# Kernel optimization log

Hardware: AMD Instinct MI355X
Metric: run time of the kernel (lower is better)

Reference implementation:

```python
import jax, jax.numpy as jnp
import numpy as np

N = 50000   # nodes
R = 4       # relation groups
E = 800000  # nnz per relation adjacency
ED = 200000 # decoded edges
H = 128     # hidden_dim
L = 64      # latent_dim
DH = 64     # decoder_hidden_dim


def setup_inputs() -> dict:
    key = jax.random.key(0)
    ks = iter(jax.random.split(key, 64))
    def nrm(shape, scale=1.0):
        return jax.random.normal(next(ks), shape, dtype=jnp.float32) * scale
    inp = {}
    inp["x_process"] = nrm((N, 62))
    inp["x_file"] = nrm((N, 37))
    inp["x_network"] = nrm((N, 37))
    def lin(prefix, din, dout):
        s = 1.0 / np.sqrt(din)
        inp[prefix + "_Ws"] = nrm((dout, din), s)
        inp[prefix + "_bs"] = nrm((dout,), s)
        inp[prefix + "_Wr"] = nrm((R, dout, din), s)
        inp[prefix + "_br"] = nrm((R, dout), s)
    lin("p1", 62, H); lin("p2", H, L)
    lin("f1", 37, H); lin("f2", H, L)
    lin("n1", 37, H); lin("n2", H, L)
    inp["gate_W"] = nrm((3, L), 1.0 / np.sqrt(L))
    inp["gate_b"] = nrm((3,), 0.1)
    inp["dec_W1"] = nrm((DH, 4 * L), 1.0 / np.sqrt(4 * L))
    inp["dec_b1"] = nrm((DH,), 0.1)
    inp["dec_W2"] = nrm((1, DH), 1.0 / np.sqrt(DH))
    inp["dec_b2"] = nrm((1,), 0.1)
    inp["adj_rows"] = jax.random.randint(next(ks), (R, E), 0, N, dtype=jnp.int32)
    inp["adj_cols"] = jax.random.randint(next(ks), (R, E), 0, N, dtype=jnp.int32)
    inp["adj_vals"] = jax.random.uniform(next(ks), (R, E), dtype=jnp.float32) * 0.1
    inp["edge_src"] = jax.random.randint(next(ks), (ED,), 0, N, dtype=jnp.int32)
    inp["edge_dst"] = jax.random.randint(next(ks), (ED,), 0, N, dtype=jnp.int32)
    return inp


def reference(x_process, x_file, x_network,
              p1_Ws, p1_bs, p1_Wr, p1_br, p2_Ws, p2_bs, p2_Wr, p2_br,
              f1_Ws, f1_bs, f1_Wr, f1_br, f2_Ws, f2_bs, f2_Wr, f2_br,
              n1_Ws, n1_bs, n1_Wr, n1_br, n2_Ws, n2_bs, n2_Wr, n2_br,
              gate_W, gate_b, dec_W1, dec_b1, dec_W2, dec_b2,
              adj_rows, adj_cols, adj_vals, edge_src, edge_dst):
    def spmm(rows, cols, vals, x):  # A @ x, A in COO: out[row] += val * x[col]
        return jax.ops.segment_sum(vals[:, None] * x[cols], rows, num_segments=N)

    def rgcn_layer(x, Ws, bs, Wr, br):
        out = x @ Ws.T + bs  # self_linear
        for r in range(R):
            out = out + spmm(adj_rows[r], adj_cols[r], adj_vals[r], x) @ Wr[r].T + br[r]
        return out / float(R + 1)

    def encoder(x, W1s, b1s, W1r, b1r, W2s, b2s, W2r, b2r):
        h = jax.nn.relu(rgcn_layer(x, W1s, b1s, W1r, b1r))
        # dropout p=0.0 / eval mode -> identity
        return rgcn_layer(h, W2s, b2s, W2r, b2r)

    z_p = encoder(x_process, p1_Ws, p1_bs, p1_Wr, p1_br, p2_Ws, p2_bs, p2_Wr, p2_br)
    z_f = encoder(x_file, f1_Ws, f1_bs, f1_Wr, f1_br, f2_Ws, f2_bs, f2_Wr, f2_br)
    z_n = encoder(x_network, n1_Ws, n1_bs, n1_Wr, n1_br, n2_Ws, n2_bs, n2_Wr, n2_br)

    # gated multi-view fusion: three Linear(latent,1) gates -> softmax over views
    scores = jnp.stack([z_p @ gate_W[0] + gate_b[0],
                        z_f @ gate_W[1] + gate_b[1],
                        z_n @ gate_W[2] + gate_b[2]], axis=1)  # [N, 3]
    alpha = jax.nn.softmax(scores, axis=1)
    z = alpha[:, 0:1] * z_p + alpha[:, 1:2] * z_f + alpha[:, 2:3] * z_n  # [N, L]

    # mlp edge decoder
    zs = z[edge_src]
    zd = z[edge_dst]
    feats = jnp.concatenate([zs, zd, zs * zd, jnp.abs(zs - zd)], axis=1)  # [ED, 4L]
    hid = jax.nn.relu(feats @ dec_W1.T + dec_b1)
    logits = (hid @ dec_W2.T + dec_b2)[:, 0]  # [ED]
    return logits
```

## Files before the change

kernel.cpp:

```cpp
#include <hip/hip_runtime.h>

#define N_NODES 50000
#define R_REL   4
#define E_NNZ   800000
#define ED_EDGES 200000
#define H_DIM   128
#define L_DIM   64

#define RN_TOTAL (R_REL * N_NODES)
#define ETOT     (R_REL * E_NNZ)

#define EPB   8192
#define NB    391
#define RBK   196
#define KBK   (R_REL * RBK)
#define HTOT  (KBK * NB)
#define SCB   300
#define MAXB  6144

#define WS_RP    0u
#define WS_HIST  800256u
#define WS_BSUM  2026496u
#define WS_CV    2030592u
#define WS_TMP   27630720u
#define WS_XALL  53230720u
#define WS_SP    72430720u
#define WS_SF    122030720u
#define WS_SN    151630720u
#define WS_HPR   181230720u
#define WS_HN    WS_TMP
#define WS_HF    WS_SP
#define WS_YSP   WS_XALL
#define WS_YSF   (WS_SP + 25600000u)
#define WS_YRP   WS_SF
#define WS_YRF   WS_SN
#define WS_YSN   WS_HPR
#define WS_YRN   WS_HF
#define WS_Z     194030720u
#define WS_PART  WS_TMP

__device__ __forceinline__ ushort f2bf(float f) {
    unsigned u = __float_as_uint(f);
    unsigned r = (u + 0x7fffu + ((u >> 16) & 1u)) >> 16;
    return (ushort)r;
}
__device__ __forceinline__ float bf2f(ushort u) {
    return __uint_as_float(((unsigned)u) << 16);
}

__global__ void cast_xall_kernel(const float* __restrict__ xp, const float* __restrict__ xf,
                                 const float* __restrict__ xn, ushort* __restrict__ xall) {
    int i = blockIdx.x * 256 + threadIdx.x;
    if (i >= N_NODES * 192) return;
    int node = i / 192, k = i - node * 192;
    float v = 0.f;
    if (k < 62) v = xp[node * 62 + k];
    else if (k >= 64 && k < 138) {
        int j = k - 64, d = j >> 1;
        v = (j & 1) ? xn[node * 37 + d] : xf[node * 37 + d];
    }
    xall[i] = f2bf(v);
}

__global__ void radix_hist_kernel(const int* __restrict__ rows, int* __restrict__ H) {
    __shared__ int hist[KBK];
    int blk = blockIdx.x, t = threadIdx.x;
    for (int i = t; i < KBK; i += 256) hist[i] = 0;
    __syncthreads();
    int base = blk * EPB;
    #pragma unroll 1
    for (int i = 0; i < EPB / 256; i++) {
        int g = base + i * 256 + t;
        if (g < ETOT) {
            int r = g / E_NNZ;
            atomicAdd(&hist[r * RBK + (rows[g] >> 8)], 1);
        }
    }
    __syncthreads();
    for (int i = t; i < KBK; i += 256) H[i * NB + blk] = hist[i];
}

__global__ void scan_part_kernel(const int* __restrict__ H, int* __restrict__ bsum) {
    __shared__ int red[256];
    int base = blockIdx.x * 1024, t = threadIdx.x;
    int s = 0;
    #pragma unroll
    for (int i = 0; i < 4; i++) {
        int idx = base + i * 256 + t;
        if (idx < HTOT) s += H[idx];
    }
    red[t] = s; __syncthreads();
    for (int d = 128; d > 0; d >>= 1) {
        if (t < d) red[t] += red[t + d];
        __syncthreads();
    }
    if (t == 0) bsum[blockIdx.x] = red[0];
}

__global__ void scan_bsum_kernel(int* __restrict__ bsum, int* __restrict__ rp) {
    __shared__ int sh[512];
    int t = threadIdx.x;
    int v = (t < SCB) ? bsum[t] : 0;
    sh[t] = v; __syncthreads();
    for (int d = 1; d < 512; d <<= 1) {
        int u = (t >= d) ? sh[t - d] : 0;
        __syncthreads();
        sh[t] += u;
        __syncthreads();
    }
    if (t < SCB) bsum[t] = sh[t] - v;
    if (t == 0) rp[RN_TOTAL] = ETOT;
}

__global__ void scan_final_kernel(int* __restrict__ H, const int* __restrict__ bsum) {
    __shared__ int sh[256];
    int base = blockIdx.x * 1024, t = threadIdx.x;
    int c[4]; int s = 0;
    #pragma unroll
    for (int i = 0; i < 4; i++) {
        int idx = base + t * 4 + i;
        c[i] = (idx < HTOT) ? H[idx] : 0;
        s += c[i];
    }
    sh[t] = s; __syncthreads();
    for (int d = 1; d < 256; d <<= 1) {
        int u = (t >= d) ? sh[t - d] : 0;
        __syncthreads();
        sh[t] += u;
        __syncthreads();
    }
    int off = bsum[blockIdx.x] + sh[t] - s;
    #pragma unroll
    for (int i = 0; i < 4; i++) {
        int idx = base + t * 4 + i;
        if (idx < HTOT) H[idx] = off;
        off += c[i];
    }
}

__global__ void radix_scatter_kernel(const int* __restrict__ rows, const int* __restrict__ cols,
                                     const float* __restrict__ vals, const int* __restrict__ H,
                                     int2* __restrict__ tmp) {
    __shared__ int cur[KBK];
    int blk = blockIdx.x, t = threadIdx.x;
    for (int i = t; i < KBK; i += 256) cur[i] = H[i * NB + blk];
    __syncthreads();
    int base = blk * EPB;
    #pragma unroll 1
    for (int i = 0; i < EPB / 256; i++) {
        int g = base + i * 256 + t;
        if (g < ETOT) {
            int r = g / E_NNZ;
            int row = rows[g];
            int b = r * RBK + (row >> 8);
            int p = atomicAdd(&cur[b], 1);
            tmp[p] = make_int2(cols[g] | ((row & 255) << 16), __float_as_int(vals[g]));
        }
    }
}

__launch_bounds__(256)
__global__ void bucket_sort_kernel(const int2* __restrict__ tmp, const int* __restrict__ H,
                                   int* __restrict__ rp, int2* __restrict__ cse) {
    __shared__ int hist[256];
    __shared__ int sc[256];
    __shared__ int cur[256];
    __shared__ int2 eb[MAXB];
    int b = blockIdx.x, t = threadIdx.x;
    int start = H[b * NB];
    int end = (b == KBK - 1) ? ETOT : H[(b + 1) * NB];
    int cnt = end - start;
    bool useLds = (cnt <= MAXB);
    hist[t] = 0;
    __syncthreads();
    for (int i = t; i < cnt; i += 256) {
        int2 e = tmp[start + i];
        if (useLds) eb[i] = e;
        atomicAdd(&hist[(e.x >> 16) & 255], 1);
    }
    __syncthreads();
    sc[t] = hist[t]; __syncthreads();
    for (int d = 1; d < 256; d <<= 1) {
        int v = (t >= d) ? sc[t - d] : 0;
        __syncthreads();
        sc[t] += v;
        __syncthreads();
    }
    int pref = sc[t] - hist[t];
    int r = b / RBK, rh = b - r * RBK;
    int grow = rh * 256 + t;
    if (grow < N_NODES) rp[r * N_NODES + grow] = start + pref;
    cur[t] = start + pref;
    __syncthreads();
    for (int i = t; i < cnt; i += 256) {
        int2 e = useLds ? eb[i] : tmp[start + i];
        int rl = (e.x >> 16) & 255;
        int p = atomicAdd(&cur[rl], 1);
        cse[p] = make_int2(e.x & 0xFFFF, e.y);
    }
}

__global__ void spmm1_all_kernel(const ushort* __restrict__ xall,
                                 const int* __restrict__ rp, const int2* __restrict__ cse,
                                 float* __restrict__ Sp, float* __restrict__ Sf,
                                 float* __restrict__ Sn) {
    int wave = threadIdx.x >> 6, lane = threadIdx.x & 63;
    int row = blockIdx.x * 4 + wave;
    if (row >= N_NODES) return;
    bool lp = lane < 62, lf = lane < 37;
    int opx = lane;
    int ofn = 64 + 2 * lane;
    for (int r = 0; r < R_REL; r++) {
        int e0 = rp[r * N_NODES + row], e1 = rp[r * N_NODES + row + 1];
        float ap = 0.f, af = 0.f, an = 0.f;
        int e = e0;
        for (; e + 4 <= e1; e += 4) {
            int2 q0 = cse[e], q1 = cse[e + 1], q2 = cse[e + 2], q3 = cse[e + 3];
            const ushort* b0 = xall + (size_t)q0.x * 192;
            const ushort* b1 = xall + (size_t)q1.x * 192;
            const ushort* b2 = xall + (size_t)q2.x * 192;
            const ushort* b3 = xall + (size_t)q3.x * 192;
            ushort  p0 = b0[opx], p1 = b1[opx], p2 = b2[opx], p3 = b3[opx];
            ushort2 u0 = *(const ushort2*)&b0[ofn];
            ushort2 u1 = *(const ushort2*)&b1[ofn];
            ushort2 u2 = *(const ushort2*)&b2[ofn];
            ushort2 u3 = *(const ushort2*)&b3[ofn];
            float v0 = __int_as_float(q0.y), v1 = __int_as_float(q1.y);
            float v2 = __int_as_float(q2.y), v3 = __int_as_float(q3.y);
            ap += v0 * bf2f(p0) + v1 * bf2f(p1) + v2 * bf2f(p2) + v3 * bf2f(p3);
            af += v0 * bf2f(u0.x) + v1 * bf2f(u1.x) + v2 * bf2f(u2.x) + v3 * bf2f(u3.x);
            an += v0 * bf2f(u0.y) + v1 * bf2f(u1.y) + v2 * bf2f(u2.y) + v3 * bf2f(u3.y);
        }
        for (; e < e1; e++) {
            int2 q = cse[e];
            const ushort* b = xall + (size_t)q.x * 192;
            float v = __int_as_float(q.y);
            ap += v * bf2f(b[opx]);
            ushort2 u = *(const ushort2*)&b[ofn];
            af += v * bf2f(u.x);
            an += v * bf2f(u.y);
        }
        if (lp) Sp[row * 248 + r * 62 + lane] = ap;
        if (lf) { Sf[row * 148 + r * 37 + lane] = af; Sn[row * 148 + r * 37 + lane] = an; }
    }
}

__launch_bounds__(256)
__global__ void gemm1_kernel(const float* __restrict__ x, const float* __restrict__ S,
                             const float* __restrict__ Ws, const float* __restrict__ bs,
                             const float* __restrict__ Wr, const float* __restrict__ br,
                             float* __restrict__ h, int din) {
    __shared__ float sA[64 * 63];
    __shared__ float sW[62 * 132];
    int t = threadIdx.x;
    int i0 = blockIdx.x * 64;
    int rg = t >> 5, cg = t & 31;
    float acc[8][4] = {};
    for (int s = 0; s < 5; s++) {
        const float* Aptr; int astride;
        if (s == 0) { Aptr = x; astride = din; }
        else        { Aptr = S + (s - 1) * din; astride = 4 * din; }
        const float* Wp = (s == 0) ? Ws : (Wr + (s - 1) * H_DIM * din);
        __syncthreads();
        for (int idx = t; idx < 64 * din; idx += 256) {
            int rr = idx / din, k = idx - rr * din;
            int grow = i0 + rr;
            sA[rr * 63 + k] = (grow < N_NODES) ? Aptr[grow * astride + k] : 0.f;
        }
        for (int idx = t; idx < H_DIM * din; idx += 256) {
            int j = idx / din, k = idx - j * din;
            sW[k * 132 + j] = Wp[j * din + k];
        }
        __syncthreads();
        for (int k = 0; k < din; k++) {
            float a[8];
            #pragma unroll
            for (int rr = 0; rr < 8; rr++) a[rr] = sA[(rg * 8 + rr) * 63 + k];
            float4 w = *(const float4*)&sW[k * 132 + cg * 4];
            #pragma unroll
            for (int rr = 0; rr < 8; rr++) {
                acc[rr][0] += a[rr] * w.x; acc[rr][1] += a[rr] * w.y;
                acc[rr][2] += a[rr] * w.z; acc[rr][3] += a[rr] * w.w;
            }
        }
    }
    int j0 = cg * 4;
    float btot[4];
    #pragma unroll
    for (int cc = 0; cc < 4; cc++) {
        float b = bs[j0 + cc];
        #pragma unroll
        for (int r = 0; r < R_REL; r++) b += br[r * H_DIM + j0 + cc];
        btot[cc] = b;
    }
    #pragma unroll
    for (int rr = 0; rr < 8; rr++) {
        int grow = i0 + rg * 8 + rr;
        if (grow < N_NODES) {
            float4 o;
            o.x = fmaxf((acc[rr][0] + btot[0]) * 0.2f, 0.f);
            o.y = fmaxf((acc[rr][1] + btot[1]) * 0.2f, 0.f);
            o.z = fmaxf((acc[rr][2] + btot[2]) * 0.2f, 0.f);
            o.w = fmaxf((acc[rr][3] + btot[3]) * 0.2f, 0.f);
            *(float4*)&h[grow * H_DIM + j0] = o;
        }
    }
}

__launch_bounds__(256)
__global__ void gemm2_kernel(const float* __restrict__ h, const float* __restrict__ Ws2,
                             const float* __restrict__ Wr2, float* __restrict__ Yself,
                             ushort* __restrict__ Yrel) {
    __shared__ float sA[128 * 65];
    __shared__ float sW[64 * 68];
    int t = threadIdx.x;
    int i0 = blockIdx.x * 128;
    int ct = blockIdx.y;
    int rg = t >> 4, cg = t & 15;
    const float* Wp = (ct == 0) ? Ws2 : (Wr2 + (ct - 1) * 64 * H_DIM);
    float acc[8][4] = {};
    for (int kc = 0; kc < 2; kc++) {
        __syncthreads();
        for (int idx = t; idx < 128 * 64; idx += 256) {
            int rr = idx >> 6, k = idx & 63;
            int grow = i0 + rr;
            sA[rr * 65 + k] = (grow < N_NODES) ? h[grow * H_DIM + kc * 64 + k] : 0.f;
        }
        for (int idx = t; idx < 64 * 64; idx += 256) {
            int j = idx >> 6, k = idx & 63;
            sW[k * 68 + j] = Wp[j * H_DIM + kc * 64 + k];
        }
        __syncthreads();
        for (int k = 0; k < 64; k++) {
            float a[8];
            #pragma unroll
            for (int rr = 0; rr < 8; rr++) a[rr] = sA[(rg * 8 + rr) * 65 + k];
            float4 w = *(const float4*)&sW[k * 68 + cg * 4];
            #pragma unroll
            for (int rr = 0; rr < 8; rr++) {
                acc[rr][0] += a[rr] * w.x; acc[rr][1] += a[rr] * w.y;
                acc[rr][2] += a[rr] * w.z; acc[rr][3] += a[rr] * w.w;
            }
        }
    }
    #pragma unroll
    for (int rr = 0; rr < 8; rr++) {
        int grow = i0 + rg * 8 + rr;
        if (grow < N_NODES) {
            if (ct == 0) {
                float4 o = make_float4(acc[rr][0], acc[rr][1], acc[rr][2], acc[rr][3]);
                *(float4*)&Yself[(size_t)grow * 64 + cg * 4] = o;
            } else {
                ushort4 o;
                o.x = f2bf(acc[rr][0]); o.y = f2bf(acc[rr][1]);
                o.z = f2bf(acc[rr][2]); o.w = f2bf(acc[rr][3]);
                *(ushort4*)&Yrel[(size_t)grow * 256 + (ct - 1) * 64 + cg * 4] = o;
            }
        }
    }
}

__global__ void spmm2z_all_kernel(const float* __restrict__ Ysp, const ushort* __restrict__ Yrp,
                                  const float* __restrict__ Ysf, const ushort* __restrict__ Yrf,
                                  const float* __restrict__ Ysn, const ushort* __restrict__ Yrn,
                                  const int* __restrict__ rp, const int2* __restrict__ cse,
                                  const float* __restrict__ p_bs, const float* __restrict__ p_br,
                                  const float* __restrict__ f_bs, const float* __restrict__ f_br,
                                  const float* __restrict__ n_bs, const float* __restrict__ n_br,
                                  const float* __restrict__ gW, const float* __restrict__ gb,
                                  float* __restrict__ z) {
    int wave = threadIdx.x >> 6, lane = threadIdx.x & 63;
    int row = blockIdx.x * 4 + wave;
    if (row >= N_NODES) return;
    float aP = Ysp[(size_t)row * 64 + lane] + p_bs[lane]
             + p_br[lane] + p_br[64 + lane] + p_br[128 + lane] + p_br[192 + lane];
    float aF = Ysf[(size_t)row * 64 + lane] + f_bs[lane]
             + f_br[lane] + f_br[64 + lane] + f_br[128 + lane] + f_br[192 + lane];
    float aN = Ysn[(size_t)row * 64 + lane] + n_bs[lane]
             + n_br[lane] + n_br[64 + lane] + n_br[128 + lane] + n_br[192 + lane];
    for (int r = 0; r < R_REL; r++) {
        int e0 = rp[r * N_NODES + row], e1 = rp[r * N_NODES + row + 1];
        const ushort* yp = Yrp + r * 64 + lane;
        const ushort* yf = Yrf + r * 64 + lane;
        const ushort* yn = Yrn + r * 64 + lane;
        int e = e0;
        for (; e + 4 <= e1; e += 4) {
            int2 q0 = cse[e], q1 = cse[e + 1], q2 = cse[e + 2], q3 = cse[e + 3];
            size_t o0 = (size_t)q0.x * 256, o1 = (size_t)q1.x * 256;
            size_t o2 = (size_t)q2.x * 256, o3 = (size_t)q3.x * 256;
            float pp0 = bf2f(yp[o0]), pp1 = bf2f(yp[o1]), pp2 = bf2f(yp[o2]), pp3 = bf2f(yp[o3]);
            float ff0 = bf2f(yf[o0]), ff1 = bf2f(yf[o1]), ff2 = bf2f(yf[o2]), ff3 = bf2f(yf[o3]);
            float nn0 = bf2f(yn[o0]), nn1 = bf2f(yn[o1]), nn2 = bf2f(yn[o2]), nn3 = bf2f(yn[o3]);
            float v0 = __int_as_float(q0.y), v1 = __int_as_float(q1.y);
            float v2 = __int_as_float(q2.y), v3 = __int_as_float(q3.y);
            aP += v0 * pp0 + v1 * pp1 + v2 * pp2 + v3 * pp3;
            aF += v0 * ff0 + v1 * ff1 + v2 * ff2 + v3 * ff3;
            aN += v0 * nn0 + v1 * nn1 + v2 * nn2 + v3 * nn3;
        }
        for (; e < e1; e++) {
            int2 q = cse[e];
            size_t o = (size_t)q.x * 256;
            float v = __int_as_float(q.y);
            aP += v * bf2f(yp[o]);
            aF += v * bf2f(yf[o]);
            aN += v * bf2f(yn[o]);
        }
    }
    aP *= 0.2f; aF *= 0.2f; aN *= 0.2f;
    float sp = aP * gW[lane], sf = aF * gW[64 + lane], sn = aN * gW[128 + lane];
    #pragma unroll
    for (int d = 32; d >= 1; d >>= 1) {
        sp += __shfl_xor(sp, d);
        sf += __shfl_xor(sf, d);
        sn += __shfl_xor(sn, d);
    }
    sp += gb[0]; sf += gb[1]; sn += gb[2];
    float m = fmaxf(sp, fmaxf(sf, sn));
    float ep = __expf(sp - m), ef = __expf(sf - m), en = __expf(sn - m);
    float inv = 1.f / (ep + ef + en);
    z[row * 64 + lane] = (ep * aP + ef * aF + en * aN) * inv;
}

__launch_bounds__(256)
__global__ void decoder5_kernel(const float* __restrict__ z, const int* __restrict__ esrc,
                                const int* __restrict__ edst, const float* __restrict__ w1,
                                const float* __restrict__ b1, const float* __restrict__ w2,
                                float* __restrict__ part) {
    __shared__ float sW1[8192];
    int t = threadIdx.x;
    int jh = blockIdx.y;
    const float* w1h = w1 + jh * 32 * 256;
    for (int i = t; i < 2048; i += 256)
        ((float4*)sW1)[i] = ((const float4*)w1h)[i];
    __syncthreads();
    int e1 = blockIdx.x * 512 + t;
    int e2 = e1 + 256;
    bool v2 = e2 < ED_EDGES;
    if (e1 >= ED_EDGES) return;
    int s1 = esrc[e1], d1 = edst[e1];
    int s2 = v2 ? esrc[e2] : s1;
    int d2 = v2 ? edst[e2] : d1;
    const float4* zs1 = (const float4*)(z + (size_t)s1 * 64);
    const float4* zd1 = (const float4*)(z + (size_t)d1 * 64);
    const float4* zs2 = (const float4*)(z + (size_t)s2 * 64);
    const float4* zd2 = (const float4*)(z + (size_t)d2 * 64);
    float hid1[32], hid2[32];
    #pragma unroll
    for (int j = 0; j < 32; j++) { hid1[j] = 0.f; hid2[j] = 0.f; }
    #pragma unroll 1
    for (int kc = 0; kc < 16; kc++) {
        float4 a1 = zs1[kc], b1v4 = zd1[kc];
        float4 a2 = zs2[kc], b2v4 = zd2[kc];
        float4 p1, q1, p2, q2;
        p1.x = a1.x * b1v4.x; q1.x = fabsf(a1.x - b1v4.x);
        p1.y = a1.y * b1v4.y; q1.y = fabsf(a1.y - b1v4.y);
        p1.z = a1.z * b1v4.z; q1.z = fabsf(a1.z - b1v4.z);
        p1.w = a1.w * b1v4.w; q1.w = fabsf(a1.w - b1v4.w);
        p2.x = a2.x * b2v4.x; q2.x = fabsf(a2.x - b2v4.x);
        p2.y = a2.y * b2v4.y; q2.y = fabsf(a2.y - b2v4.y);
        p2.z = a2.z * b2v4.z; q2.z = fabsf(a2.z - b2v4.z);
        p2.w = a2.w * b2v4.w; q2.w = fabsf(a2.w - b2v4.w);
        const float* wb0 = sW1 + kc * 4;
        #pragma unroll
        for (int j = 0; j < 32; j++) {
            const float* wr = wb0 + j * 256;
            float4 wa = *(const float4*)(wr);
            float4 wbv = *(const float4*)(wr + 64);
            float4 wc = *(const float4*)(wr + 128);
            float4 wd = *(const float4*)(wr + 192);
            hid1[j] += a1.x * wa.x + a1.y * wa.y + a1.z * wa.z + a1.w * wa.w
                     + b1v4.x * wbv.x + b1v4.y * wbv.y + b1v4.z * wbv.z + b1v4.w * wbv.w
                     + p1.x * wc.x + p1.y * wc.y + p1.z * wc.z + p1.w * wc.w
                     + q1.x * wd.x + q1.y * wd.y + q1.z * wd.z + q1.w * wd.w;
            hid2[j] += a2.x * wa.x + a2.y * wa.y + a2.z * wa.z + a2.w * wa.w
                     + b2v4.x * wbv.x + b2v4.y * wbv.y + b2v4.z * wbv.z + b2v4.w * wbv.w
                     + p2.x * wc.x + p2.y * wc.y + p2.z * wc.z + p2.w * wc.w
                     + q2.x * wd.x + q2.y * wd.y + q2.z * wd.z + q2.w * wd.w;
        }
    }
    float lg1 = 0.f, lg2 = 0.f;
    #pragma unroll
    for (int j = 0; j < 32; j++) {
        int gj = jh * 32 + j;
        float bj = b1[gj], wj = w2[gj];
        lg1 += fmaxf(hid1[j] + bj, 0.f) * wj;
        lg2 += fmaxf(hid2[j] + bj, 0.f) * wj;
    }
    part[(size_t)jh * ED_EDGES + e1] = lg1;
    if (v2) part[(size_t)jh * ED_EDGES + e2] = lg2;
}

__global__ void dec_combine_kernel(const float* __restrict__ part, const float* __restrict__ b2,
                                   float* __restrict__ out) {
    int e = blockIdx.x * 256 + threadIdx.x;
    if (e < ED_EDGES) out[e] = part[e] + part[ED_EDGES + e] + b2[0];
}

extern "C" void kernel_launch(void* const* d_in, const int* in_sizes, int n_in,
                              void* d_out, int out_size, void* d_ws, size_t ws_size,
                              hipStream_t stream) {
    const float* x_p = (const float*)d_in[0];
    const float* x_f = (const float*)d_in[1];
    const float* x_n = (const float*)d_in[2];
    const float* p1_Ws = (const float*)d_in[3];  const float* p1_bs = (const float*)d_in[4];
    const float* p1_Wr = (const float*)d_in[5];  const float* p1_br = (const float*)d_in[6];
    const float* p2_Ws = (const float*)d_in[7];  const float* p2_bs = (const float*)d_in[8];
    const float* p2_Wr = (const float*)d_in[9];  const float* p2_br = (const float*)d_in[10];
    const float* f1_Ws = (const float*)d_in[11]; const float* f1_bs = (const float*)d_in[12];
    const float* f1_Wr = (const float*)d_in[13]; const float* f1_br = (const float*)d_in[14];
    const float* f2_Ws = (const float*)d_in[15]; const float* f2_bs = (const float*)d_in[16];
    const float* f2_Wr = (const float*)d_in[17]; const float* f2_br = (const float*)d_in[18];
    const float* n1_Ws = (const float*)d_in[19]; const float* n1_bs = (const float*)d_in[20];
    const float* n1_Wr = (const float*)d_in[21]; const float* n1_br = (const float*)d_in[22];
    const float* n2_Ws = (const float*)d_in[23]; const float* n2_bs = (const float*)d_in[24];
    const float* n2_Wr = (const float*)d_in[25]; const float* n2_br = (const float*)d_in[26];
    const float* gate_W = (const float*)d_in[27]; const float* gate_b = (const float*)d_in[28];
    const float* dec_W1 = (const float*)d_in[29]; const float* dec_b1 = (const float*)d_in[30];
    const float* dec_W2 = (const float*)d_in[31]; const float* dec_b2 = (const float*)d_in[32];
    const int*   adj_rows = (const int*)d_in[33];
    const int*   adj_cols = (const int*)d_in[34];
    const float* adj_vals = (const float*)d_in[35];
    const int*   edge_src = (const int*)d_in[36];
    const int*   edge_dst = (const int*)d_in[37];

    char* ws = (char*)d_ws;
    int*    rp   = (int*)(ws + WS_RP);
    int*    H    = (int*)(ws + WS_HIST);
    int*    bsum = (int*)(ws + WS_BSUM);
    int2*   cse  = (int2*)(ws + WS_CV);
    int2*   tmp  = (int2*)(ws + WS_TMP);
    ushort* xall = (ushort*)(ws + WS_XALL);
    float*  S_p = (float*)(ws + WS_SP);
    float*  S_f = (float*)(ws + WS_SF);
    float*  S_n = (float*)(ws + WS_SN);
    float*  h_p = (float*)(ws + WS_HPR);
    float*  h_f = (float*)(ws + WS_HF);
    float*  h_n = (float*)(ws + WS_HN);
    float*  Ys_p = (float*)(ws + WS_YSP);  ushort* Yr_p = (ushort*)(ws + WS_YRP);
    float*  Ys_f = (float*)(ws + WS_YSF);  ushort* Yr_f = (ushort*)(ws + WS_YRF);
    float*  Ys_n = (float*)(ws + WS_YSN);  ushort* Yr_n = (ushort*)(ws + WS_YRN);
    float*  z    = (float*)(ws + WS_Z);
    float*  part = (float*)(ws + WS_PART);
    float*  out  = (float*)d_out;

    cast_xall_kernel<<<(N_NODES * 192 + 255) / 256, 256, 0, stream>>>(x_p, x_f, x_n, xall);

    radix_hist_kernel<<<NB, 256, 0, stream>>>(adj_rows, H);
    scan_part_kernel<<<SCB, 256, 0, stream>>>(H, bsum);
    scan_bsum_kernel<<<1, 512, 0, stream>>>(bsum, rp);
    scan_final_kernel<<<SCB, 256, 0, stream>>>(H, bsum);
    radix_scatter_kernel<<<NB, 256, 0, stream>>>(adj_rows, adj_cols, adj_vals, H, tmp);
    bucket_sort_kernel<<<KBK, 256, 0, stream>>>(tmp, H, rp, cse);

    spmm1_all_kernel<<<N_NODES / 4, 256, 0, stream>>>(xall, rp, cse, S_p, S_f, S_n);

    int g1 = (N_NODES + 63) / 64;
    gemm1_kernel<<<g1, 256, 0, stream>>>(x_p, S_p, p1_Ws, p1_bs, p1_Wr, p1_br, h_p, 62);
    gemm1_kernel<<<g1, 256, 0, stream>>>(x_f, S_f, f1_Ws, f1_bs, f1_Wr, f1_br, h_f, 37);
    gemm1_kernel<<<g1, 256, 0, stream>>>(x_n, S_n, n1_Ws, n1_bs, n1_Wr, n1_br, h_n, 37);

    dim3 g2((N_NODES + 127) / 128, 5);
    gemm2_kernel<<<g2, 256, 0, stream>>>(h_p, p2_Ws, p2_Wr, Ys_p, Yr_p);
    gemm2_kernel<<<g2, 256, 0, stream>>>(h_f, f2_Ws, f2_Wr, Ys_f, Yr_f);
    gemm2_kernel<<<g2, 256, 0, stream>>>(h_n, n2_Ws, n2_Wr, Ys_n, Yr_n);

    spmm2z_all_kernel<<<N_NODES / 4, 256, 0, stream>>>(
        Ys_p, Yr_p, Ys_f, Yr_f, Ys_n, Yr_n, rp, cse,
        p2_bs, p2_br, f2_bs, f2_br, n2_bs, n2_br, gate_W, gate_b, z);

    dim3 gd((ED_EDGES + 511) / 512, 2);
    decoder5_kernel<<<gd, 256, 0, stream>>>(
        z, edge_src, edge_dst, dec_W1, dec_b1, dec_W2, part);
    dec_combine_kernel<<<(ED_EDGES + 255) / 256, 256, 0, stream>>>(part, dec_b2, out);
}
```

Baseline: 1.406 ms.

## Split wavefront into half-waves processing two edges with wider vector gathers

Both SpMM kernels now split each 64-lane wave into two 32-lane halves, each handling alternate nonzeros and loading two or four bf16 features per lane instead of one. The partial sums are combined with a cross-half shuffle. This raises the number of independent gathers in flight per wave and widens each load, aimed at the latency of the gather loads. A small kernel now precomputes the summed second-layer biases once instead of per row, which adds one launch and leaves half the lanes idle during stores.

Measured after the change: 1.401 ms. About the same (-0.3%).

```diff
diff --git a/kernel.cpp b/kernel.cpp
--- a/kernel.cpp
+++ b/kernel.cpp
@@ -21,6 +21,7 @@
 #define WS_RP    0u
 #define WS_HIST  800256u
 #define WS_BSUM  2026496u
+#define WS_BIAS3 (WS_BSUM + 2048u)
 #define WS_CV    2030592u
 #define WS_TMP   27630720u
 #define WS_XALL  53230720u
@@ -207,41 +208,58 @@
     int wave = threadIdx.x >> 6, lane = threadIdx.x & 63;
     int row = blockIdx.x * 4 + wave;
     if (row >= N_NODES) return;
-    bool lp = lane < 62, lf = lane < 37;
-    int opx = lane;
-    int ofn = 64 + 2 * lane;
+    int h = lane >> 5, j = lane & 31;
+    unsigned d0 = 2u * (unsigned)j;
+    unsigned po = d0;
+    unsigned fo = 64u + 2u * d0;
     for (int r = 0; r < R_REL; r++) {
         int e0 = rp[r * N_NODES + row], e1 = rp[r * N_NODES + row + 1];
-        float ap = 0.f, af = 0.f, an = 0.f;
+        float ap0 = 0.f, ap1 = 0.f, af0 = 0.f, af1 = 0.f, an0 = 0.f, an1 = 0.f;
         int e = e0;
-        for (; e + 4 <= e1; e += 4) {
-            int2 q0 = cse[e], q1 = cse[e + 1], q2 = cse[e + 2], q3 = cse[e + 3];
-            const ushort* b0 = xall + (size_t)q0.x * 192;
-            const ushort* b1 = xall + (size_t)q1.x * 192;
-            const ushort* b2 = xall + (size_t)q2.x * 192;
-            const ushort* b3 = xall + (size_t)q3.x * 192;
-            ushort  p0 = b0[opx], p1 = b1[opx], p2 = b2[opx], p3 = b3[opx];
-            ushort2 u0 = *(const ushort2*)&b0[ofn];
-            ushort2 u1 = *(const ushort2*)&b1[ofn];
-            ushort2 u2 = *(const ushort2*)&b2[ofn];
-            ushort2 u3 = *(const ushort2*)&b3[ofn];
-            float v0 = __int_as_float(q0.y), v1 = __int_as_float(q1.y);
-            float v2 = __int_as_float(q2.y), v3 = __int_as_float(q3.y);
-            ap += v0 * bf2f(p0) + v1 * bf2f(p1) + v2 * bf2f(p2) + v3 * bf2f(p3);
-            af += v0 * bf2f(u0.x) + v1 * bf2f(u1.x) + v2 * bf2f(u2.x) + v3 * bf2f(u3.x);
-            an += v0 * bf2f(u0.y) + v1 * bf2f(u1.y) + v2 * bf2f(u2.y) + v3 * bf2f(u3.y);
-        }
-        for (; e < e1; e++) {
-            int2 q = cse[e];
-            const ushort* b = xall + (size_t)q.x * 192;
-            float v = __int_as_float(q.y);
-            ap += v * bf2f(b[opx]);
-            ushort2 u = *(const ushort2*)&b[ofn];
-            af += v * bf2f(u.x);
-            an += v * bf2f(u.y);
-        }
-        if (lp) Sp[row * 248 + r * 62 + lane] = ap;
-        if (lf) { Sf[row * 148 + r * 37 + lane] = af; Sn[row * 148 + r * 37 + lane] = an; }
+        for (; e + 8 <= e1; e += 8) {
+            int2 qA = cse[e + h],     qB = cse[e + 2 + h];
+            int2 qC = cse[e + 4 + h], qD = cse[e + 6 + h];
+            unsigned bA = (unsigned)qA.x * 192u, bB = (unsigned)qB.x * 192u;
+            unsigned bC = (unsigned)qC.x * 192u, bD = (unsigned)qD.x * 192u;
+            ushort2 pA = *(const ushort2*)(xall + bA + po);
+            ushort2 pB = *(const ushort2*)(xall + bB + po);
+            ushort2 pC = *(const ushort2*)(xall + bC + po);
+            ushort2 pD = *(const ushort2*)(xall + bD + po);
+            ushort4 uA = *(const ushort4*)(xall + bA + fo);
+            ushort4 uB = *(const ushort4*)(xall + bB + fo);
+            ushort4 uC = *(const ushort4*)(xall + bC + fo);
+            ushort4 uD = *(const ushort4*)(xall + bD + fo);
+            float vA = __int_as_float(qA.y), vB = __int_as_float(qB.y);
+            float vC = __int_as_float(qC.y), vD = __int_as_float(qD.y);
+            ap0 += vA * bf2f(pA.x) + vB * bf2f(pB.x) + vC * bf2f(pC.x) + vD * bf2f(pD.x);
+            ap1 += vA * bf2f(pA.y) + vB * bf2f(pB.y) + vC * bf2f(pC.y) + vD * bf2f(pD.y);
+            af0 += vA * bf2f(uA.x) + vB * bf2f(uB.x) + vC * bf2f(uC.x) + vD * bf2f(uD.x);
+            an0 += vA * bf2f(uA.y) + vB * bf2f(uB.y) + vC * bf2f(uC.y) + vD * bf2f(uD.y);
+            af1 += vA * bf2f(uA.z) + vB * bf2f(uB.z) + vC * bf2f(uC.z) + vD * bf2f(uD.z);
+            an1 += vA * bf2f(uA.w) + vB * bf2f(uB.w) + vC * bf2f(uC.w) + vD * bf2f(uD.w);
+        }
+        for (; e < e1; e += 2) {
+            int idx = e + h;
+            int2 q = cse[idx < e1 ? idx : e1 - 1];
+            float v = (idx < e1) ? __int_as_float(q.y) : 0.f;
+            unsigned b = (unsigned)q.x * 192u;
+            ushort2 p = *(const ushort2*)(xall + b + po);
+            ushort4 u = *(const ushort4*)(xall + b + fo);
+            ap0 += v * bf2f(p.x); ap1 += v * bf2f(p.y);
+            af0 += v * bf2f(u.x); an0 += v * bf2f(u.y);
+            af1 += v * bf2f(u.z); an1 += v * bf2f(u.w);
+        }
+        ap0 += __shfl_xor(ap0, 32); ap1 += __shfl_xor(ap1, 32);
+        af0 += __shfl_xor(af0, 32); af1 += __shfl_xor(af1, 32);
+        an0 += __shfl_xor(an0, 32); an1 += __shfl_xor(an1, 32);
+        if (h == 0) {
+            int d = (int)d0;
+            if (d < 62) *(float2*)(Sp + row * 248 + r * 62 + d) = make_float2(ap0, ap1);
+            float* sfp = Sf + row * 148 + r * 37;
+            float* snp = Sn + row * 148 + r * 37;
+            if (d < 37) { sfp[d] = af0; snp[d] = an0; }
+            if (d < 36) { sfp[d + 1] = af1; snp[d + 1] = an1; }
+        }
     }
 }
 
@@ -360,56 +378,91 @@
     }
 }
 
+__global__ void bias_prep_kernel(const float* __restrict__ pbs, const float* __restrict__ pbr,
+                                 const float* __restrict__ fbs, const float* __restrict__ fbr,
+                                 const float* __restrict__ nbs, const float* __restrict__ nbr,
+                                 float* __restrict__ bias3) {
+    int t = threadIdx.x;
+    if (t >= 192) return;
+    int view = t >> 6, d = t & 63;
+    const float* bs = (view == 0) ? pbs : (view == 1) ? fbs : nbs;
+    const float* br = (view == 0) ? pbr : (view == 1) ? fbr : nbr;
+    float b = bs[d];
+    #pragma unroll
+    for (int r = 0; r < R_REL; r++) b += br[r * 64 + d];
+    bias3[t] = b;
+}
+
 __global__ void spmm2z_all_kernel(const float* __restrict__ Ysp, const ushort* __restrict__ Yrp,
                                   const float* __restrict__ Ysf, const ushort* __restrict__ Yrf,
                                   const float* __restrict__ Ysn, const ushort* __restrict__ Yrn,
                                   const int* __restrict__ rp, const int2* __restrict__ cse,
-                                  const float* __restrict__ p_bs, const float* __restrict__ p_br,
-                                  const float* __restrict__ f_bs, const float* __restrict__ f_br,
-                                  const float* __restrict__ n_bs, const float* __restrict__ n_br,
+                                  const float* __restrict__ bias3,
                                   const float* __restrict__ gW, const float* __restrict__ gb,
                                   float* __restrict__ z) {
     int wave = threadIdx.x >> 6, lane = threadIdx.x & 63;
     int row = blockIdx.x * 4 + wave;
     if (row >= N_NODES) return;
-    float aP = Ysp[(size_t)row * 64 + lane] + p_bs[lane]
-             + p_br[lane] + p_br[64 + lane] + p_br[128 + lane] + p_br[192 + lane];
-    float aF = Ysf[(size_t)row * 64 + lane] + f_bs[lane]
-             + f_br[lane] + f_br[64 + lane] + f_br[128 + lane] + f_br[192 + lane];
-    float aN = Ysn[(size_t)row * 64 + lane] + n_bs[lane]
-             + n_br[lane] + n_br[64 + lane] + n_br[128 + lane] + n_br[192 + lane];
+    int h = lane >> 5, j = lane & 31;
+    unsigned d0 = 2u * (unsigned)j;
+    float aP0 = 0.f, aP1 = 0.f, aF0 = 0.f, aF1 = 0.f, aN0 = 0.f, aN1 = 0.f;
     for (int r = 0; r < R_REL; r++) {
         int e0 = rp[r * N_NODES + row], e1 = rp[r * N_NODES + row + 1];
-        const ushort* yp = Yrp + r * 64 + lane;
-        const ushort* yf = Yrf + r * 64 + lane;
-        const ushort* yn = Yrn + r * 64 + lane;
+        unsigned ofs = (unsigned)(r * 64) + d0;
         int e = e0;
-        for (; e + 4 <= e1; e += 4) {
-            int2 q0 = cse[e], q1 = cse[e + 1], q2 = cse[e + 2], q3 = cse[e + 3];
-            size_t o0 = (size_t)q0.x * 256, o1 = (size_t)q1.x * 256;
-            size_t o2 = (size_t)q2.x * 256, o3 = (size_t)q3.x * 256;
-            float pp0 = bf2f(yp[o0]), pp1 = bf2f(yp[o1]), pp2 = bf2f(yp[o2]), pp3 = bf2f(yp[o3]);
-            float ff0 = bf2f(yf[o0]), ff1 = bf2f(yf[o1]), ff2 = bf2f(yf[o2]), ff3 = bf2f(yf[o3]);
-            float nn0 = bf2f(yn[o0]), nn1 = bf2f(yn[o1]), nn2 = bf2f(yn[o2]), nn3 = bf2f(yn[o3]);
-            float v0 = __int_as_float(q0.y), v1 = __int_as_float(q1.y);
-            float v2 = __int_as_float(q2.y), v3 = __int_as_float(q3.y);
-            aP += v0 * pp0 + v1 * pp1 + v2 * pp2 + v3 * pp3;
-            aF += v0 * ff0 + v1 * ff1 + v2 * ff2 + v3 * ff3;
-            aN += v0 * nn0 + v1 * nn1 + v2 * nn2 + v3 * nn3;
-        }
-        for (; e < e1; e++) {
-            int2 q = cse[e];
-            size_t o = (size_t)q.x * 256;
-            float v = __int_as_float(q.y);
-            aP += v * bf2f(yp[o]);
-            aF += v * bf2f(yf[o]);
-            aN += v * bf2f(yn[o]);
-        }
-    }
-    aP *= 0.2f; aF *= 0.2f; aN *= 0.2f;
-    float sp = aP * gW[lane], sf = aF * gW[64 + lane], sn = aN * gW[128 + lane];
-    #pragma unroll
-    for (int d = 32; d >= 1; d >>= 1) {
+        for (; e + 8 <= e1; e += 8) {
+            int2 qA = cse[e + h],     qB = cse[e + 2 + h];
+            int2 qC = cse[e + 4 + h], qD = cse[e + 6 + h];
+            unsigned oA = (unsigned)qA.x * 256u + ofs;
+            unsigned oB = (unsigned)qB.x * 256u + ofs;
+            unsigned oC = (unsigned)qC.x * 256u + ofs;
+            unsigned oD = (unsigned)qD.x * 256u + ofs;
+            ushort2 pA = *(const ushort2*)(Yrp + oA), pB = *(const ushort2*)(Yrp + oB);
+            ushort2 pC = *(const ushort2*)(Yrp + oC), pD = *(const ushort2*)(Yrp + oD);
+            ushort2 fA = *(const ushort2*)(Yrf + oA), fB = *(const ushort2*)(Yrf + oB);
+            ushort2 fC = *(const ushort2*)(Yrf + oC), fD = *(const ushort2*)(Yrf + oD);
+            ushort2 nA = *(const ushort2*)(Yrn + oA), nB = *(const ushort2*)(Yrn + oB);
+            ushort2 nC = *(const ushort2*)(Yrn + oC), nD = *(const ushort2*)(Yrn + oD);
+            float vA = __int_as_float(qA.y), vB = __int_as_float(qB.y);
+            float vC = __int_as_float(qC.y), vD = __int_as_float(qD.y);
+            aP0 += vA * bf2f(pA.x) + vB * bf2f(pB.x) + vC * bf2f(pC.x) + vD * bf2f(pD.x);
+            aP1 += vA * bf2f(pA.y) + vB * bf2f(pB.y) + vC * bf2f(pC.y) + vD * bf2f(pD.y);
+            aF0 += vA * bf2f(fA.x) + vB * bf2f(fB.x) + vC * bf2f(fC.x) + vD * bf2f(fD.x);
+            aF1 += vA * bf2f(fA.y) + vB * bf2f(fB.y) + vC * bf2f(fC.y) + vD * bf2f(fD.y);
+            aN0 += vA * bf2f(nA.x) + vB * bf2f(nB.x) + vC * bf2f(nC.x) + vD * bf2f(nD.x);
+            aN1 += vA * bf2f(nA.y) + vB * bf2f(nB.y) + vC * bf2f(nC.y) + vD * bf2f(nD.y);
+        }
+        for (; e < e1; e += 2) {
+            int idx = e + h;
+            int2 q = cse[idx < e1 ? idx : e1 - 1];
+            float v = (idx < e1) ? __int_as_float(q.y) : 0.f;
+            unsigned o = (unsigned)q.x * 256u + ofs;
+            ushort2 p = *(const ushort2*)(Yrp + o);
+            ushort2 f = *(const ushort2*)(Yrf + o);
+            ushort2 n = *(const ushort2*)(Yrn + o);
+            aP0 += v * bf2f(p.x); aP1 += v * bf2f(p.y);
+            aF0 += v * bf2f(f.x); aF1 += v * bf2f(f.y);
+            aN0 += v * bf2f(n.x); aN1 += v * bf2f(n.y);
+        }
+    }
+    aP0 += __shfl_xor(aP0, 32); aP1 += __shfl_xor(aP1, 32);
+    aF0 += __shfl_xor(aF0, 32); aF1 += __shfl_xor(aF1, 32);
+    aN0 += __shfl_xor(aN0, 32); aN1 += __shfl_xor(aN1, 32);
+    size_t rb = (size_t)row * 64 + d0;
+    float2 ysp = *(const float2*)(Ysp + rb);
+    float2 ysf = *(const float2*)(Ysf + rb);
+    float2 ysn = *(const float2*)(Ysn + rb);
+    aP0 = (aP0 + ysp.x + bias3[d0]) * 0.2f;
+    aP1 = (aP1 + ysp.y + bias3[d0 + 1]) * 0.2f;
+    aF0 = (aF0 + ysf.x + bias3[64 + d0]) * 0.2f;
+    aF1 = (aF1 + ysf.y + bias3[64 + d0 + 1]) * 0.2f;
+    aN0 = (aN0 + ysn.x + bias3[128 + d0]) * 0.2f;
+    aN1 = (aN1 + ysn.y + bias3[128 + d0 + 1]) * 0.2f;
+    float sp = aP0 * gW[d0] + aP1 * gW[d0 + 1];
+    float sf = aF0 * gW[64 + d0] + aF1 * gW[64 + d0 + 1];
+    float sn = aN0 * gW[128 + d0] + aN1 * gW[128 + d0 + 1];
+    #pragma unroll
+    for (int d = 16; d >= 1; d >>= 1) {
         sp += __shfl_xor(sp, d);
         sf += __shfl_xor(sf, d);
         sn += __shfl_xor(sn, d);
@@ -418,7 +471,12 @@
     float m = fmaxf(sp, fmaxf(sf, sn));
     float ep = __expf(sp - m), ef = __expf(sf - m), en = __expf(sn - m);
     float inv = 1.f / (ep + ef + en);
-    z[row * 64 + lane] = (ep * aP + ef * aF + en * aN) * inv;
+    if (h == 0) {
+        float2 zo;
+        zo.x = (ep * aP0 + ef * aF0 + en * aN0) * inv;
+        zo.y = (ep * aP1 + ef * aF1 + en * aN1) * inv;
+        *(float2*)(z + rb) = zo;
+    }
 }
 
 __launch_bounds__(256)
@@ -527,6 +585,7 @@
     int*    rp   = (int*)(ws + WS_RP);
     int*    H    = (int*)(ws + WS_HIST);
     int*    bsum = (int*)(ws + WS_BSUM);
+    float*  bias3 = (float*)(ws + WS_BIAS3);
     int2*   cse  = (int2*)(ws + WS_CV);
     int2*   tmp  = (int2*)(ws + WS_TMP);
     ushort* xall = (ushort*)(ws + WS_XALL);
@@ -564,9 +623,9 @@
     gemm2_kernel<<<g2, 256, 0, stream>>>(h_f, f2_Ws, f2_Wr, Ys_f, Yr_f);
     gemm2_kernel<<<g2, 256, 0, stream>>>(h_n, n2_Ws, n2_Wr, Ys_n, Yr_n);
 
+    bias_prep_kernel<<<1, 192, 0, stream>>>(p2_bs, p2_br, f2_bs, f2_br, n2_bs, n2_br, bias3);
     spmm2z_all_kernel<<<N_NODES / 4, 256, 0, stream>>>(
-        Ys_p, Yr_p, Ys_f, Yr_f, Ys_n, Yr_n, rp, cse,
-        p2_bs, p2_br, f2_bs, f2_br, n2_bs, n2_br, gate_W, gate_b, z);
+        Ys_p, Yr_p, Ys_f, Yr_f, Ys_n, Yr_n, rp, cse, bias3, gate_W, gate_b, z);
 
     dim3 gd((ED_EDGES + 511) / 512, 2);
     decoder5_kernel<<<gd, 256, 0, stream>>>(
```
